# Performance work log

Measured on AMD Instinct MI355X. Metric: run time of the kernel, lower is better.

## Reference

```python
import jax, jax.numpy as jnp
import numpy as np

MARGIN = 0.1
B, D, C = 16384, 4096, 10

def setup_inputs() -> dict:
    key = jax.random.key(0)
    k1, k2, k3, k4 = jax.random.split(key, 4)
    pred = jax.random.normal(k1, (B, D), dtype=jnp.float32)
    anchors = jax.random.normal(k2, (C, D), dtype=jnp.float32)
    clss = jax.random.randint(k3, (B,), 0, C, dtype=jnp.int64)
    neg_offset = jax.random.randint(k4, (B,), 0, 9, dtype=jnp.int64)
    return {"pred": pred, "anchors": anchors, "clss": clss, "neg_offset": neg_offset}

def reference(pred, anchors, clss, neg_offset):
    # negative class: uniform over the 9 classes != clss
    neg_clss = (clss + 1 + neg_offset % 9) % C  # [B]
    t_feat = anchors[clss]        # [B, D] positive prototypes (gather)
    n_feat = anchors[neg_clss]    # [B, D] negative prototypes (gather)
    # per-sample MSE over feature dim (nn.MSELoss default = mean)
    mse_pos = jnp.mean((pred - t_feat) ** 2, axis=-1)  # [B]
    mse_neg = jnp.mean((pred - n_feat) ** 2, axis=-1)  # [B]
    loss = jnp.mean(mse_pos - mse_neg + MARGIN)
    return loss
```

## Files before the change

### kernel.cpp

```cpp
#include <hip/hip_runtime.h>

#define BB 16384
#define DD 4096
#define CC 10
#define MARGIN 0.1
#define NBLK (BB / 4)

__global__ __launch_bounds__(256) void tl_main(
        const float* __restrict__ pred,
        const float* __restrict__ anchors,
        const int*   __restrict__ clss,
        const int*   __restrict__ neg_offset,
        double*      __restrict__ partial) {
    const int wave = threadIdx.x >> 6;
    const int lane = threadIdx.x & 63;
    const int row  = blockIdx.x * 4 + wave;

    const int cls = clss[row];
    const int neg = (cls + 1 + (neg_offset[row] % 9)) % CC;

    const float4* p4 = (const float4*)pred    + (size_t)row * (DD / 4);
    const float4* t4 = (const float4*)anchors + (size_t)cls * (DD / 4);
    const float4* n4 = (const float4*)anchors + (size_t)neg * (DD / 4);

    float s = 0.0f;
    #pragma unroll
    for (int i = 0; i < (DD / 4) / 64; ++i) {
        const int j = i * 64 + lane;
        float4 p = p4[j];
        float4 t = t4[j];
        float4 n = n4[j];
        float dp, dn;
        dp = p.x - t.x; dn = p.x - n.x; s += dp * dp - dn * dn;
        dp = p.y - t.y; dn = p.y - n.y; s += dp * dp - dn * dn;
        dp = p.z - t.z; dn = p.z - n.z; s += dp * dp - dn * dn;
        dp = p.w - t.w; dn = p.w - n.w; s += dp * dp - dn * dn;
    }

    #pragma unroll
    for (int off = 32; off > 0; off >>= 1)
        s += __shfl_down(s, off, 64);

    __shared__ float wsum[4];
    if (lane == 0) wsum[wave] = s;
    __syncthreads();

    if (threadIdx.x == 0) {
        partial[blockIdx.x] = (double)wsum[0] + (double)wsum[1]
                            + (double)wsum[2] + (double)wsum[3];
    }
}

__global__ __launch_bounds__(256) void tl_reduce(
        const double* __restrict__ partial,
        float* __restrict__ out) {
    const int tid = threadIdx.x;
    double s = 0.0;
    #pragma unroll
    for (int i = 0; i < NBLK / 256; ++i)
        s += partial[i * 256 + tid];

    __shared__ double sh[256];
    sh[tid] = s;
    __syncthreads();
    #pragma unroll
    for (int stride = 128; stride > 0; stride >>= 1) {
        if (tid < stride) sh[tid] += sh[tid + stride];
        __syncthreads();
    }
    if (tid == 0)
        out[0] = (float)(MARGIN + sh[0] / ((double)BB * (double)DD));
}

extern "C" void kernel_launch(void* const* d_in, const int* in_sizes, int n_in,
                              void* d_out, int out_size, void* d_ws, size_t ws_size,
                              hipStream_t stream) {
    const float* pred       = (const float*)d_in[0];
    const float* anchors    = (const float*)d_in[1];
    const int*   clss       = (const int*)d_in[2];
    const int*   neg_offset = (const int*)d_in[3];
    float*  out     = (float*)d_out;
    double* partial = (double*)d_ws;

    hipLaunchKernelGGL(tl_main, dim3(NBLK), dim3(256), 0, stream,
                       pred, anchors, clss, neg_offset, partial);
    hipLaunchKernelGGL(tl_reduce, dim3(1), dim3(256), 0, stream, partial, out);
}
```

Baseline: 359.6 us.

## Precompute anchor difference vectors per class pair to reduce gather traffic

```diff
diff --git a/kernel.cpp b/kernel.cpp
--- a/kernel.cpp
+++ b/kernel.cpp
@@ -3,52 +3,85 @@
 #define BB 16384
 #define DD 4096
 #define CC 10
+#define NPAIR 90
 #define MARGIN 0.1
 #define NBLK (BB / 4)
 
+
+__global__ __launch_bounds__(256) void tl_prep(
+        const float* __restrict__ anchors,
+        float*  __restrict__ diffs,
+        double* __restrict__ consts) {
+    const int pair = blockIdx.x;
+    const int c   = pair / 9;
+    const int o   = pair % 9;
+    const int neg = (c + 1 + o) % CC;
+
+    const float4* t4 = (const float4*)anchors + (size_t)c   * (DD / 4);
+    const float4* n4 = (const float4*)anchors + (size_t)neg * (DD / 4);
+    float4* d4 = (float4*)diffs + (size_t)pair * (DD / 4);
+
+    double acc = 0.0;
+    for (int i = threadIdx.x; i < DD / 4; i += 256) {
+        float4 t = t4[i];
+        float4 n = n4[i];
+        float4 d;
+        d.x = t.x - n.x; d.y = t.y - n.y; d.z = t.z - n.z; d.w = t.w - n.w;
+        d4[i] = d;
+        acc += (double)t.x * t.x - (double)n.x * n.x;
+        acc += (double)t.y * t.y - (double)n.y * n.y;
+        acc += (double)t.z * t.z - (double)n.z * n.z;
+        acc += (double)t.w * t.w - (double)n.w * n.w;
+    }
+
+    __shared__ double sh[256];
+    sh[threadIdx.x] = acc;
+    __syncthreads();
+    #pragma unroll
+    for (int stride = 128; stride > 0; stride >>= 1) {
+        if (threadIdx.x < stride) sh[threadIdx.x] += sh[threadIdx.x + stride];
+        __syncthreads();
+    }
+    if (threadIdx.x == 0) consts[pair] = sh[0];
+}
+
 __global__ __launch_bounds__(256) void tl_main(
         const float* __restrict__ pred,
-        const float* __restrict__ anchors,
         const int*   __restrict__ clss,
         const int*   __restrict__ neg_offset,
-        double*      __restrict__ partial) {
+        const float* __restrict__ diffs,
+        const double* __restrict__ consts,
+        double* __restrict__ partial) {
     const int wave = threadIdx.x >> 6;
     const int lane = threadIdx.x & 63;
     const int row  = blockIdx.x * 4 + wave;
 
-    const int cls = clss[row];
-    const int neg = (cls + 1 + (neg_offset[row] % 9)) % CC;
+    const int cls  = clss[row];
+    const int pair = cls * 9 + (neg_offset[row] % 9);
 
-    const float4* p4 = (const float4*)pred    + (size_t)row * (DD / 4);
-    const float4* t4 = (const float4*)anchors + (size_t)cls * (DD / 4);
-    const float4* n4 = (const float4*)anchors + (size_t)neg * (DD / 4);
+    const float4* p4 = (const float4*)pred  + (size_t)row  * (DD / 4);
+    const float4* d4 = (const float4*)diffs + (size_t)pair * (DD / 4);
 
     float s = 0.0f;
-    #pragma unroll
+    #pragma unroll 4
     for (int i = 0; i < (DD / 4) / 64; ++i) {
         const int j = i * 64 + lane;
         float4 p = p4[j];
-        float4 t = t4[j];
-        float4 n = n4[j];
-        float dp, dn;
-        dp = p.x - t.x; dn = p.x - n.x; s += dp * dp - dn * dn;
-        dp = p.y - t.y; dn = p.y - n.y; s += dp * dp - dn * dn;
-        dp = p.z - t.z; dn = p.z - n.z; s += dp * dp - dn * dn;
-        dp = p.w - t.w; dn = p.w - n.w; s += dp * dp - dn * dn;
+        float4 d = d4[j];
+        s += p.x * d.x + p.y * d.y + p.z * d.z + p.w * d.w;
     }
 
     #pragma unroll
     for (int off = 32; off > 0; off >>= 1)
         s += __shfl_down(s, off, 64);
 
-    __shared__ float wsum[4];
-    if (lane == 0) wsum[wave] = s;
+    __shared__ double wsum[4];
+    if (lane == 0)
+        wsum[wave] = consts[pair] - 2.0 * (double)s;
     __syncthreads();
 
-    if (threadIdx.x == 0) {
-        partial[blockIdx.x] = (double)wsum[0] + (double)wsum[1]
-                            + (double)wsum[2] + (double)wsum[3];
-    }
+    if (threadIdx.x == 0)
+        partial[blockIdx.x] = wsum[0] + wsum[1] + wsum[2] + wsum[3];
 }
 
 __global__ __launch_bounds__(256) void tl_reduce(
@@ -79,10 +112,16 @@
     const float* anchors    = (const float*)d_in[1];
     const int*   clss       = (const int*)d_in[2];
     const int*   neg_offset = (const int*)d_in[3];
-    float*  out     = (float*)d_out;
-    double* partial = (double*)d_ws;
+    float* out = (float*)d_out;
 
+    char* ws = (char*)d_ws;
+    double* partial = (double*)(ws);
+    double* consts  = (double*)(ws + (32u << 10));
+    float*  diffs   = (float*)(ws + (64u << 10));
+
+    hipLaunchKernelGGL(tl_prep, dim3(NPAIR), dim3(256), 0, stream,
+                       anchors, diffs, consts);
     hipLaunchKernelGGL(tl_main, dim3(NBLK), dim3(256), 0, stream,
-                       pred, anchors, clss, neg_offset, partial);
+                       pred, clss, neg_offset, diffs, consts, partial);
     hipLaunchKernelGGL(tl_reduce, dim3(1), dim3(256), 0, stream, partial, out);
 }
```

After: 362.9 us. No clear change (+0.9%).
